# Kernel tuning notes

Hardware: AMD Instinct MI355X
Metric: run time of the kernel (lower is better)

## Reference

```python
import jax, jax.numpy as jnp
import numpy as np

BETA = 15.0   # soft-max temperature used by the soft morphology (logsumexp pooling)
EPS = 1e-5    # BatchNorm eps
BIG = 1e4     # padding value so padded taps vanish in logsumexp


def _soft_morph(x, w, dilation, op):
    """Channel-wise soft morphology. x: (B,C,H,W), w: (C,k,k).
    dilation (erode=False): out = (1/b)*logsumexp_i b*(w_i + x_i)
    erosion: out = -(1/b)*logsumexp_i b*(w_i - x_i)
    """
    C, k, _ = w.shape
    B, _, H, W = x.shape
    pad = dilation * (k - 1) // 2
    pad_val = -BIG if op == 'dil' else BIG
    xp = jnp.pad(x, ((0, 0), (0, 0), (pad, pad), (pad, pad)), constant_values=pad_val)
    taps = []
    for i in range(k):
        for j in range(k):
            patch = xp[:, :, i * dilation:i * dilation + H, j * dilation:j * dilation + W]
            wij = w[:, i, j][None, :, None, None]
            taps.append(wij + patch if op == 'dil' else wij - patch)
    s = jnp.stack(taps, 0)  # (k*k, B, C, H, W)
    out = jax.nn.logsumexp(s * BETA, axis=0) / BETA
    return out if op == 'dil' else -out


def _opening(x, w_ero, w_dil, dilation):
    return _soft_morph(_soft_morph(x, w_ero, dilation, 'ero'), w_dil, dilation, 'dil')


def _bn(x, g, b, m, v):
    scale = (g / jnp.sqrt(v + EPS))[None, :, None, None]
    return (x - m[None, :, None, None]) * scale + b[None, :, None, None]


def setup_inputs() -> dict:
    key = jax.random.key(0)
    ks = jax.random.split(key, 8)
    B, C, H, W, k = 4, 64, 256, 256, 3
    x = jax.random.normal(ks[0], (B, C, H, W), dtype=jnp.float32)
    we = jax.random.normal(ks[1], (4, C, k, k), dtype=jnp.float32) * 0.1   # erosion SEs per branch
    wd = jax.random.normal(ks[2], (4, C, k, k), dtype=jnp.float32) * 0.1   # dilation SEs per branch
    bn_g = jax.random.normal(ks[3], (4, C), dtype=jnp.float32) * 0.1 + 1.0
    bn_b = jax.random.normal(ks[4], (4, C), dtype=jnp.float32) * 0.1
    bn_m = jnp.zeros((4, C), dtype=jnp.float32)
    bn_v = jnp.ones((4, C), dtype=jnp.float32)
    conv_w = jax.random.normal(ks[5], (C, 4 * C), dtype=jnp.float32) * (1.0 / np.sqrt(4 * C))
    bnf_g = jax.random.normal(ks[6], (C,), dtype=jnp.float32) * 0.1 + 1.0
    bnf_b = jax.random.normal(ks[7], (C,), dtype=jnp.float32) * 0.1
    bnf_m = jnp.zeros((C,), dtype=jnp.float32)
    bnf_v = jnp.ones((C,), dtype=jnp.float32)
    return {"x": x, "we": we, "wd": wd, "bn_g": bn_g, "bn_b": bn_b, "bn_m": bn_m,
            "bn_v": bn_v, "conv_w": conv_w, "bnf_g": bnf_g, "bnf_b": bnf_b,
            "bnf_m": bnf_m, "bnf_v": bnf_v}


def reference(x, we, wd, bn_g, bn_b, bn_m, bn_v, conv_w, bnf_g, bnf_b, bnf_m, bnf_v):
    outs = []
    for d in range(4):  # dilations 1..4
        y = _opening(x, we[d], wd[d], d + 1)
        outs.append(jax.nn.relu(_bn(y, bn_g[d], bn_b[d], bn_m[d], bn_v[d])))
    cat = jnp.concatenate(outs, axis=1)             # (B, 4C, H, W)
    z = jnp.einsum('oc,bchw->bohw', conv_w, cat)    # 1x1 conv, no bias
    z = jax.nn.relu(_bn(z, bnf_g, bnf_b, bnf_m, bnf_v))
    return z  # Dropout2d is identity in eval mode
```

## Files before the change

### kernel.cpp

```cpp
#include <hip/hip_runtime.h>
#include <hip/hip_fp16.h>
#include <math.h>


constexpr int C_ = 64, H_ = 256, W_ = 256;
constexpr int HW = H_ * W_;
constexpr float BIGV = 10000.0f;
constexpr float EPSV = 1e-5f;
constexpr float KL2E = 21.64042561333445f;
constexpr float C1   = 0.046209812037329684f;

typedef __attribute__((ext_vector_type(8))) _Float16 half8v;
typedef __attribute__((ext_vector_type(4))) float f32x4;

__device__ _Float16 g_wh[64 * 256];
__device__ float g_scale[64];
__device__ float g_shift[64];

__global__ __launch_bounds__(256) void prep(
    const float* __restrict__ cw, const float* __restrict__ g,
    const float* __restrict__ bb, const float* __restrict__ bm,
    const float* __restrict__ bv)
{
    int i = blockIdx.x * 256 + threadIdx.x;
    g_wh[i] = (_Float16)cw[i];
    if (i < 64) {
        float s = g[i] * rsqrtf(bv[i] + EPSV);
        g_scale[i] = s;
        g_shift[i] = bb[i] - bm[i] * s;
    }
}

__global__ __launch_bounds__(256) void morph_all(
    const float* __restrict__ x, const float* __restrict__ we,
    const float* __restrict__ wd, const float* __restrict__ bng,
    const float* __restrict__ bnb, const float* __restrict__ bnm,
    const float* __restrict__ bnv, _Float16* __restrict__ cat)
{
    __shared__ __align__(16) float xs[80 * 52];
    __shared__ __align__(16) float es[72 * 44];
    __shared__ float wsh[9], wdsh[9];
    const int tid = threadIdx.x;
    const int tileW = blockIdx.x & 7, tileH = blockIdx.x >> 3;
    const int c = blockIdx.y, b = blockIdx.z;
    const int h0 = tileH * 64, w0 = tileW * 32;
    const float* xc = x + (b * C_ + c) * HW;

    for (int u = tid; u < 960; u += 256) {
        int r = u / 12, q4 = (u - r * 12) * 4;
        int gh = h0 - 8 + r, gw = w0 - 8 + q4;
        int ch = min(max(gh, 0), 255), cwi = min(max(gw, 0), 252);
        const float4 v = *(const float4*)&xc[ch * W_ + cwi];
        bool ok = ((unsigned)gh < 256u) && ((unsigned)gw < 253u);
        float4 sv;
        sv.x = ok ? __builtin_amdgcn_exp2f(-KL2E * v.x) : 0.f;
        sv.y = ok ? __builtin_amdgcn_exp2f(-KL2E * v.y) : 0.f;
        sv.z = ok ? __builtin_amdgcn_exp2f(-KL2E * v.z) : 0.f;
        sv.w = ok ? __builtin_amdgcn_exp2f(-KL2E * v.w) : 0.f;
        *(float4*)&xs[r * 52 + q4] = sv;
    }

    #pragma unroll
    for (int d = 0; d < 4; d++) {
        const int D = d + 1;

        __syncthreads();
        if (tid < 9)
            wsh[tid] = __builtin_amdgcn_exp2f(KL2E * we[(d * C_ + c) * 9 + tid]);
        else if (tid >= 16 && tid < 25)
            wdsh[tid - 16] = __builtin_amdgcn_exp2f(KL2E * wd[(d * C_ + c) * 9 + tid - 16]);
        __syncthreads();

        float w9[9];
        #pragma unroll
        for (int i = 0; i < 9; i++) w9[i] = wsh[i];

        const int row0 = 4 - D, NG = (64 + 2 * D) * 5;
        for (int g = tid; g < NG; g += 256) {
            int gr = g / 5;
            int ra = row0 + gr, qa0 = (g - gr * 5) * 8;
            f32x4 xw[3][4];
            #pragma unroll
            for (int i = 0; i < 3; i++) {
                const f32x4* xr = (const f32x4*)&xs[(ra + 4 + (i - 1) * D) * 52 + qa0];
                xw[i][0] = xr[0]; xw[i][1] = xr[1]; xw[i][2] = xr[2]; xw[i][3] = xr[3];
            }
            bool rowok = (unsigned)(h0 + ra - 4) < 256u;
            const int gw0 = w0 + qa0 - 4;
            f32x4 gv[2];
            #pragma unroll
            for (int p = 0; p < 8; p++) {
                float s = 0.f;
                #pragma unroll
                for (int i = 0; i < 3; i++)
                    #pragma unroll
                    for (int j = 0; j < 3; j++) {
                        const int wi = (4 - D) + p + j * D;
                        s = fmaf(w9[i * 3 + j], xw[i][wi >> 2][wi & 3], s);
                    }
                float gwv = __builtin_amdgcn_rcpf(fmaxf(s, 1e-38f));
                bool ok = rowok && ((unsigned)(gw0 + p) < 256u);
                gv[p >> 2][p & 3] = ok ? gwv : 0.f;
            }
            f32x4* ep = (f32x4*)&es[ra * 44 + qa0];
            ep[0] = gv[0]; ep[1] = gv[1];
        }

        float wd9[9];
        #pragma unroll
        for (int i = 0; i < 9; i++) wd9[i] = wdsh[i];
        const int bc = d * C_ + c;
        float scale = bng[bc] * rsqrtf(bnv[bc] + EPSV);
        float shift = bnb[bc] - bnm[bc] * scale;
        float cs = C1 * scale;

        __syncthreads();

        {
            const int dr = tid >> 2, dq0 = (tid & 3) * 8;
            f32x4 ew[3][4];
            #pragma unroll
            for (int i = 0; i < 3; i++) {
                const f32x4* er = (const f32x4*)&es[(dr + 4 + (i - 1) * D) * 44 + dq0];
                ew[i][0] = er[0]; ew[i][1] = er[1]; ew[i][2] = er[2]; ew[i][3] = er[3];
            }
            half8v hv;
            #pragma unroll
            for (int p = 0; p < 8; p++) {
                float s = 0.f;
                #pragma unroll
                for (int i = 0; i < 3; i++)
                    #pragma unroll
                    for (int j = 0; j < 3; j++) {
                        const int wi = (4 - D) + p + j * D;
                        s = fmaf(wd9[i * 3 + j], ew[i][wi >> 2][wi & 3], s);
                    }
                float y = __builtin_amdgcn_logf(fmaxf(s, 1e-38f)) * cs + shift;
                hv[p] = (_Float16)fmaxf(0.f, y);
            }
            *(half8v*)&cat[((size_t)((b * 4 + d) * C_ + c)) * HW
                           + (h0 + dr) * W_ + (w0 + dq0)] = hv;
        }
    }
}

__global__ __launch_bounds__(256) void conv_mfma(
    const _Float16* __restrict__ cat, float* __restrict__ out)
{
    __shared__ _Float16 T[2][32 * 258];
    const int tid = threadIdx.x;
    const int lane = tid & 63, wave = tid >> 6;
    const int m = lane & 15, quad = lane >> 4;
    const int b = blockIdx.y;
    const int px0 = blockIdx.x * 256;
    const _Float16* catb = cat + (size_t)b * 256 * HW + px0;

    const int cl = tid >> 3;
    const int px8 = (tid & 7) * 8;

    f32x4 acc[4][4];
    #pragma unroll
    for (int ot = 0; ot < 4; ot++)
        #pragma unroll
        for (int pt = 0; pt < 4; pt++)
            acc[ot][pt] = (f32x4){0.f, 0.f, 0.f, 0.f};

    half8v sv[2][4];
    #pragma unroll
    for (int p = 0; p < 4; p++) {
        sv[0][p] = *(const half8v*)&catb[(size_t)cl * HW + p * 64 + px8];
        sv[1][p] = *(const half8v*)&catb[(size_t)(32 + cl) * HW + p * 64 + px8];
    }

    #pragma unroll
    for (int kc = 0; kc < 8; kc++) {
        const int buf = kc & 1;
        const int c0 = kc * 32;
        #pragma unroll
        for (int p = 0; p < 4; p++) {
            uint* tw = (uint*)&T[buf][cl * 258 + p * 64 + px8];
            const uint* svw = (const uint*)&sv[buf][p];
            tw[0] = svw[0]; tw[1] = svw[1]; tw[2] = svw[2]; tw[3] = svw[3];
        }
        if (kc < 6) {
            #pragma unroll
            for (int p = 0; p < 4; p++)
                sv[buf][p] = *(const half8v*)&catb[(size_t)(c0 + 64 + cl) * HW + p * 64 + px8];
        }
        __syncthreads();

        half8v a0 = *(const half8v*)&g_wh[(0  + m) * 256 + c0 + quad * 8];
        half8v a1 = *(const half8v*)&g_wh[(16 + m) * 256 + c0 + quad * 8];
        half8v a2 = *(const half8v*)&g_wh[(32 + m) * 256 + c0 + quad * 8];
        half8v a3 = *(const half8v*)&g_wh[(48 + m) * 256 + c0 + quad * 8];

        #pragma unroll
        for (int pt = 0; pt < 4; pt++) {
            const int pxl = wave * 64 + pt * 16 + m;
            const int tb = quad * 8 * 258 + pxl;
            half8v bf;
            #pragma unroll
            for (int j = 0; j < 8; j++)
                bf[j] = T[buf][tb + j * 258];
            acc[0][pt] = __builtin_amdgcn_mfma_f32_16x16x32_f16(a0, bf, acc[0][pt], 0, 0, 0);
            acc[1][pt] = __builtin_amdgcn_mfma_f32_16x16x32_f16(a1, bf, acc[1][pt], 0, 0, 0);
            acc[2][pt] = __builtin_amdgcn_mfma_f32_16x16x32_f16(a2, bf, acc[2][pt], 0, 0, 0);
            acc[3][pt] = __builtin_amdgcn_mfma_f32_16x16x32_f16(a3, bf, acc[3][pt], 0, 0, 0);
        }
    }

    #pragma unroll
    for (int ot = 0; ot < 4; ot++)
        #pragma unroll
        for (int reg = 0; reg < 4; reg++) {
            const int o = ot * 16 + quad * 4 + reg;
            const float sc = g_scale[o], sh = g_shift[o];
            float* ob = out + ((size_t)(b * 64 + o)) * HW + px0;
            #pragma unroll
            for (int pt = 0; pt < 4; pt++) {
                const int pxl = wave * 64 + pt * 16 + m;
                ob[pxl] = fmaxf(0.f, acc[ot][pt][reg] * sc + sh);
            }
        }
}

extern "C" void kernel_launch(void* const* d_in, const int* in_sizes, int n_in,
                              void* d_out, int out_size, void* d_ws, size_t ws_size,
                              hipStream_t stream)
{
    const float* x   = (const float*)d_in[0];
    const float* we  = (const float*)d_in[1];
    const float* wd  = (const float*)d_in[2];
    const float* bng = (const float*)d_in[3];
    const float* bnb = (const float*)d_in[4];
    const float* bnm = (const float*)d_in[5];
    const float* bnv = (const float*)d_in[6];
    const float* cw  = (const float*)d_in[7];
    const float* fg  = (const float*)d_in[8];
    const float* fb  = (const float*)d_in[9];
    const float* fm  = (const float*)d_in[10];
    const float* fv  = (const float*)d_in[11];
    float* out = (float*)d_out;
    _Float16* cat = (_Float16*)d_ws;

    prep<<<64, 256, 0, stream>>>(cw, fg, fb, fm, fv);
    morph_all<<<dim3(32, 64, 4), 256, 0, stream>>>(x, we, wd, bng, bnb, bnm, bnv, cat);
    conv_mfma<<<dim3(256, 4), 256, 0, stream>>>(cat, out);
}
```

Baseline: 263.2 us.

## Widen morph tiles to 64 columns and compute 16 outputs per thread

The morphology kernel's spatial tile grows from 64x32 to 64x64, which halves the grid and shrinks the share of halo loads and exp work per output. Each thread now computes 16 consecutive outputs from a 24-wide register window, so more outputs reuse each LDS read. The SE weights are read straight from global memory into registers, dropping the shared-memory weight staging and one barrier per dilation. In exchange the kernel uses more LDS and registers, which may lower occupancy, and the smaller grid gives less parallelism.

```diff
diff --git a/kernel.cpp b/kernel.cpp
--- a/kernel.cpp
+++ b/kernel.cpp
@@ -5,7 +5,6 @@
 
 constexpr int C_ = 64, H_ = 256, W_ = 256;
 constexpr int HW = H_ * W_;
-constexpr float BIGV = 10000.0f;
 constexpr float EPSV = 1e-5f;
 constexpr float KL2E = 21.64042561333445f;
 constexpr float C1   = 0.046209812037329684f;
@@ -37,17 +36,16 @@
     const float* __restrict__ bnb, const float* __restrict__ bnm,
     const float* __restrict__ bnv, _Float16* __restrict__ cat)
 {
-    __shared__ __align__(16) float xs[80 * 52];
-    __shared__ __align__(16) float es[72 * 44];
-    __shared__ float wsh[9], wdsh[9];
+    __shared__ __align__(16) float xs[80 * 92];
+    __shared__ __align__(16) float es[72 * 84];
     const int tid = threadIdx.x;
-    const int tileW = blockIdx.x & 7, tileH = blockIdx.x >> 3;
+    const int tileW = blockIdx.x & 3, tileH = blockIdx.x >> 2;
     const int c = blockIdx.y, b = blockIdx.z;
-    const int h0 = tileH * 64, w0 = tileW * 32;
+    const int h0 = tileH * 64, w0 = tileW * 64;
     const float* xc = x + (b * C_ + c) * HW;
 
-    for (int u = tid; u < 960; u += 256) {
-        int r = u / 12, q4 = (u - r * 12) * 4;
+    for (int u = tid; u < 1600; u += 256) {
+        int r = u / 20, q4 = (u - r * 20) * 4;
         int gh = h0 - 8 + r, gw = w0 - 8 + q4;
         int ch = min(max(gh, 0), 255), cwi = min(max(gw, 0), 252);
         const float4 v = *(const float4*)&xc[ch * W_ + cwi];
@@ -57,58 +55,19 @@
         sv.y = ok ? __builtin_amdgcn_exp2f(-KL2E * v.y) : 0.f;
         sv.z = ok ? __builtin_amdgcn_exp2f(-KL2E * v.z) : 0.f;
         sv.w = ok ? __builtin_amdgcn_exp2f(-KL2E * v.w) : 0.f;
-        *(float4*)&xs[r * 52 + q4] = sv;
+        *(float4*)&xs[r * 92 + q4] = sv;
     }
 
     #pragma unroll
     for (int d = 0; d < 4; d++) {
         const int D = d + 1;
 
-        __syncthreads();
-        if (tid < 9)
-            wsh[tid] = __builtin_amdgcn_exp2f(KL2E * we[(d * C_ + c) * 9 + tid]);
-        else if (tid >= 16 && tid < 25)
-            wdsh[tid - 16] = __builtin_amdgcn_exp2f(KL2E * wd[(d * C_ + c) * 9 + tid - 16]);
-        __syncthreads();
-
-        float w9[9];
-        #pragma unroll
-        for (int i = 0; i < 9; i++) w9[i] = wsh[i];
-
-        const int row0 = 4 - D, NG = (64 + 2 * D) * 5;
-        for (int g = tid; g < NG; g += 256) {
-            int gr = g / 5;
-            int ra = row0 + gr, qa0 = (g - gr * 5) * 8;
-            f32x4 xw[3][4];
-            #pragma unroll
-            for (int i = 0; i < 3; i++) {
-                const f32x4* xr = (const f32x4*)&xs[(ra + 4 + (i - 1) * D) * 52 + qa0];
-                xw[i][0] = xr[0]; xw[i][1] = xr[1]; xw[i][2] = xr[2]; xw[i][3] = xr[3];
-            }
-            bool rowok = (unsigned)(h0 + ra - 4) < 256u;
-            const int gw0 = w0 + qa0 - 4;
-            f32x4 gv[2];
-            #pragma unroll
-            for (int p = 0; p < 8; p++) {
-                float s = 0.f;
-                #pragma unroll
-                for (int i = 0; i < 3; i++)
-                    #pragma unroll
-                    for (int j = 0; j < 3; j++) {
-                        const int wi = (4 - D) + p + j * D;
-                        s = fmaf(w9[i * 3 + j], xw[i][wi >> 2][wi & 3], s);
-                    }
-                float gwv = __builtin_amdgcn_rcpf(fmaxf(s, 1e-38f));
-                bool ok = rowok && ((unsigned)(gw0 + p) < 256u);
-                gv[p >> 2][p & 3] = ok ? gwv : 0.f;
-            }
-            f32x4* ep = (f32x4*)&es[ra * 44 + qa0];
-            ep[0] = gv[0]; ep[1] = gv[1];
-        }
-
-        float wd9[9];
-        #pragma unroll
-        for (int i = 0; i < 9; i++) wd9[i] = wdsh[i];
+        float w9[9], wd9[9];
+        #pragma unroll
+        for (int i = 0; i < 9; i++) {
+            w9[i]  = __builtin_amdgcn_exp2f(KL2E * we[(d * C_ + c) * 9 + i]);
+            wd9[i] = __builtin_amdgcn_exp2f(KL2E * wd[(d * C_ + c) * 9 + i]);
+        }
         const int bc = d * C_ + c;
         float scale = bng[bc] * rsqrtf(bnv[bc] + EPSV);
         float shift = bnb[bc] - bnm[bc] * scale;
@@ -116,30 +75,76 @@
 
         __syncthreads();
 
+        for (int g = tid; g < 360; g += 256) {
+            const int col = g / 72;
+            const int row = g - col * 72;
+            const int qa0 = col * 16;
+            float s16[16];
+            #pragma unroll
+            for (int p = 0; p < 16; p++) s16[p] = 0.f;
+            #pragma unroll
+            for (int i = 0; i < 3; i++) {
+                const f32x4* xr = (const f32x4*)&xs[(row + 4 + (i - 1) * D) * 92 + qa0];
+                f32x4 xw[6];
+                #pragma unroll
+                for (int k = 0; k < 6; k++) xw[k] = xr[k];
+                #pragma unroll
+                for (int j = 0; j < 3; j++) {
+                    const float wv = w9[i * 3 + j];
+                    #pragma unroll
+                    for (int p = 0; p < 16; p++) {
+                        const int wi = (4 - D) + p + j * D;
+                        s16[p] = fmaf(wv, xw[wi >> 2][wi & 3], s16[p]);
+                    }
+                }
+            }
+            const bool rowok = (unsigned)(h0 + row - 4) < 256u;
+            const int gw0 = w0 + qa0 - 4;
+            f32x4 ev[4];
+            #pragma unroll
+            for (int p = 0; p < 16; p++) {
+                float gv = __builtin_amdgcn_rcpf(fmaxf(s16[p], 1e-38f));
+                bool ok = rowok && ((unsigned)(gw0 + p) < 256u);
+                ev[p >> 2][p & 3] = ok ? gv : 0.f;
+            }
+            f32x4* ep = (f32x4*)&es[row * 84 + qa0];
+            ep[0] = ev[0]; ep[1] = ev[1]; ep[2] = ev[2]; ep[3] = ev[3];
+        }
+
+        __syncthreads();
+
         {
-            const int dr = tid >> 2, dq0 = (tid & 3) * 8;
-            f32x4 ew[3][4];
+            const int dr = tid >> 2, dq0 = (tid & 3) * 16;
+            float s16[16];
+            #pragma unroll
+            for (int p = 0; p < 16; p++) s16[p] = 0.f;
             #pragma unroll
             for (int i = 0; i < 3; i++) {
-                const f32x4* er = (const f32x4*)&es[(dr + 4 + (i - 1) * D) * 44 + dq0];
-                ew[i][0] = er[0]; ew[i][1] = er[1]; ew[i][2] = er[2]; ew[i][3] = er[3];
-            }
-            half8v hv;
-            #pragma unroll
-            for (int p = 0; p < 8; p++) {
-                float s = 0.f;
-                #pragma unroll
-                for (int i = 0; i < 3; i++)
+                const f32x4* er = (const f32x4*)&es[(dr + 4 + (i - 1) * D) * 84 + dq0];
+                f32x4 ew[6];
+                #pragma unroll
+                for (int k = 0; k < 6; k++) ew[k] = er[k];
+                #pragma unroll
+                for (int j = 0; j < 3; j++) {
+                    const float wv = wd9[i * 3 + j];
                     #pragma unroll
-                    for (int j = 0; j < 3; j++) {
+                    for (int p = 0; p < 16; p++) {
                         const int wi = (4 - D) + p + j * D;
-                        s = fmaf(wd9[i * 3 + j], ew[i][wi >> 2][wi & 3], s);
+                        s16[p] = fmaf(wv, ew[wi >> 2][wi & 3], s16[p]);
                     }
-                float y = __builtin_amdgcn_logf(fmaxf(s, 1e-38f)) * cs + shift;
-                hv[p] = (_Float16)fmaxf(0.f, y);
-            }
-            *(half8v*)&cat[((size_t)((b * 4 + d) * C_ + c)) * HW
-                           + (h0 + dr) * W_ + (w0 + dq0)] = hv;
+                }
+            }
+            half8v hv0, hv1;
+            #pragma unroll
+            for (int p = 0; p < 16; p++) {
+                float y = __builtin_amdgcn_logf(fmaxf(s16[p], 1e-38f)) * cs + shift;
+                y = fmaxf(0.f, y);
+                if (p < 8) hv0[p] = (_Float16)y; else hv1[p - 8] = (_Float16)y;
+            }
+            _Float16* cp = &cat[((size_t)((b * 4 + d) * C_ + c)) * HW
+                                + (h0 + dr) * W_ + (w0 + dq0)];
+            *(half8v*)cp = hv0;
+            *(half8v*)(cp + 8) = hv1;
         }
     }
 }
@@ -244,6 +249,6 @@
     _Float16* cat = (_Float16*)d_ws;
 
     prep<<<64, 256, 0, stream>>>(cw, fg, fb, fm, fv);
-    morph_all<<<dim3(32, 64, 4), 256, 0, stream>>>(x, we, wd, bng, bnb, bnm, bnv, cat);
+    morph_all<<<dim3(16, 64, 4), 256, 0, stream>>>(x, we, wd, bng, bnb, bnm, bnv, cat);
     conv_mfma<<<dim3(256, 4), 256, 0, stream>>>(cat, out);
 }
```

After: 253.6 us. 1.04x faster.
